# Optimization experiments

Measured on AMD Instinct MI355X. Metric: run time of the kernel, lower is better.

## Reference

```python
import jax, jax.numpy as jnp
import numpy as np

N, R, E, H, D_MAX = 1024, 8192, 1024, 4, 48
DH = E // H
P_EDGE = 16.0 / R  # average in-degree ~16


def setup_inputs() -> dict:
    key = jax.random.key(0)
    ks = jax.random.split(key, 6)
    s = 0.02
    return {
        "target": jax.random.normal(ks[0], (N, E), jnp.float32),
        "source": jax.random.normal(ks[1], (R, E), jnp.float32),
        "adj": (jax.random.uniform(ks[2], (N, R)) < P_EDGE).astype(jnp.float32),
        "W_trans": jax.random.normal(ks[3], (E, E), jnp.float32) * s,
        "b_trans": jnp.zeros((E,), jnp.float32),
        "in_proj_w": jax.random.normal(ks[4], (3 * E, E), jnp.float32) * s,
        "in_proj_b": jnp.zeros((3 * E,), jnp.float32),
        "out_w": jax.random.normal(ks[5], (E, E), jnp.float32) * s,
        "out_b": jnp.zeros((E,), jnp.float32),
        "unit_id": 0,
    }


def reference(target, source, adj, W_trans, b_trans, in_proj_w, in_proj_b, out_w, out_b, unit_id):
    # source = relu(trans_fc(source))
    src = jax.nn.relu(source @ W_trans.T + b_trans)  # [R, E]

    # build padded neighbor index lists (torch loops per node; here vectorized)
    deg = adj.sum(axis=1).astype(jnp.int32)                # [N]
    order = jnp.argsort(-adj, axis=1)[:, :D_MAX]           # stable: 1-columns first, ascending col idx
    valid = jnp.arange(D_MAX)[None, :] < deg[:, None]      # [N, D] True = real neighbor
    neigh = jnp.where(valid, order, 0)                     # pad with index 0 (masked, like torch)
    kv_in = src[neigh]                                     # [N, D, E] gathered neighbor feats

    # nn.MultiheadAttention: q=target (len-1 query), k=v=padded neighbors
    Wq, Wk, Wv = jnp.split(in_proj_w, 3, axis=0)
    bq, bk, bv = jnp.split(in_proj_b, 3)
    q = (target @ Wq.T + bq).reshape(-1, H, DH)            # [N, H, dh]
    k = (kv_in @ Wk.T + bk).reshape(-1, D_MAX, H, DH)      # [N, D, H, dh]
    v = (kv_in @ Wv.T + bv).reshape(-1, D_MAX, H, DH)

    scores = jnp.einsum('nhd,nkhd->nhk', q, k) / np.float32(np.sqrt(DH))  # [N, H, D]
    # key_padding_mask: padded slots -> -inf; give zero-degree nodes one dummy
    # unmasked slot so softmax stays finite (their output is zeroed below)
    safe_valid = valid.at[:, 0].set(valid[:, 0] | (deg == 0))
    scores = jnp.where(safe_valid[:, None, :], scores, -jnp.inf)
    attn = jax.nn.softmax(scores, axis=-1)
    out = jnp.einsum('nhk,nkhd->nhd', attn, v).reshape(-1, E)
    out = out @ out_w.T + out_b

    # scatter back: inactive (degree-0) nodes stay zero, like att_res_padded
    return jnp.where((deg > 0)[:, None], out, jnp.zeros((), out.dtype))
```

## Files before the change

kernel.cpp:

```cpp
#include <hip/hip_runtime.h>

#define N_NODES 1024
#define R_SRC   8192
#define E_DIM   1024
#define H_HEADS 4
#define DH_DIM  256
#define D_MAXN  48
#define NCONVB  1024

typedef __attribute__((ext_vector_type(8))) short short8;
typedef __attribute__((ext_vector_type(4))) float f32x4;

__device__ __forceinline__ unsigned short f2bf(float f) {
    unsigned u = __float_as_uint(f);
    unsigned r = u + 0x7fffu + ((u >> 16) & 1u);
    return (unsigned short)(r >> 16);
}
__device__ __forceinline__ float bf2f(unsigned short b) {
    return __uint_as_float(((unsigned)b) << 16);
}
__device__ __forceinline__ void gload16(const void* g, void* l) {
    __builtin_amdgcn_global_load_lds(
        (const __attribute__((address_space(1))) unsigned int*)g,
        (__attribute__((address_space(3))) unsigned int*)l,
        16, 0, 0);
}
template<int N> __device__ __forceinline__ void vwait() {
    if constexpr (N == 8)       asm volatile("s_waitcnt vmcnt(8)" ::: "memory");
    else if constexpr (N == 6)  asm volatile("s_waitcnt vmcnt(6)" ::: "memory");
    else if constexpr (N == 4)  asm volatile("s_waitcnt vmcnt(4)" ::: "memory");
    else if constexpr (N == 2)  asm volatile("s_waitcnt vmcnt(2)" ::: "memory");
    else                        asm volatile("s_waitcnt vmcnt(0)" ::: "memory");
}

struct GD {
    const unsigned short* A;
    const unsigned short* B;
    const float* bias;
    void* C;
    int N, K, nbx, relu, outbf;
    const int* rowmask;
};

template<int BM, int BN>
__global__ __launch_bounds__(512) void gemm_t(GD d0, GD d1, int split)
{
    constexpr int AI = BM / 64;
    constexpr int BI = BN / 64;
    constexpr int VN = AI + BI;
    constexpr int FM = BM / 32;
    constexpr int FN = BN / 64;

    __shared__ __align__(16) unsigned short lds[3][(BM + BN) * 64];

    int bid = blockIdx.x;
    const int nwg = gridDim.x;
    bid = (bid & 7) * (nwg >> 3) + (bid >> 3);

    GD d; int q;
    if (bid < split) { d = d0; q = bid; }
    else             { d = d1; q = bid - split; }
    const int m0 = (q / d.nbx) * BM;
    const int n0 = (q % d.nbx) * BN;
    const int K  = d.K;

    const int t = threadIdx.x;
    const int w = t >> 6, l = t & 63;
    const int wm = w >> 2, wn = w & 3;

    const int trow = t >> 3, tkc = t & 7;
    const int tswz = tkc ^ (trow & 7);
    const unsigned short* gA[AI];
    const unsigned short* gB[BI];
#pragma unroll
    for (int i = 0; i < AI; ++i)
        gA[i] = d.A + (size_t)(m0 + i * 64 + trow) * K + tswz * 8;
#pragma unroll
    for (int i = 0; i < BI; ++i)
        gB[i] = d.B + (size_t)(n0 + i * 64 + trow) * K + tswz * 8;

    f32x4 acc[FM][FN] = {};

    auto STAGE = [&](int c, int kt) {
        const int ko = kt * 64;
#pragma unroll
        for (int i = 0; i < AI; ++i)
            gload16(gA[i] + ko, &lds[c][(i * 512 + t) * 8]);
#pragma unroll
        for (int i = 0; i < BI; ++i)
            gload16(gB[i] + ko, &lds[c][BM * 64 + (i * 512 + t) * 8]);
    };

    const int nt = K / 64;
    STAGE(0, 0);
    STAGE(1, 1);
    vwait<VN>();
    __builtin_amdgcn_s_barrier();

    const int lr = l & 15, hi = l >> 4;
    const int rsw = l & 7;
    const int cs0 = ((0 + hi) ^ rsw) * 8;
    const int cs1 = ((4 + hi) ^ rsw) * 8;
    const int abase = (wm * (BM / 2) + lr) * 64;
    const int bbase = BM * 64 + (wn * 64 + lr) * 64;

    for (int kt = 0; kt < nt; ++kt) {
        const int cur = kt % 3;
        if (kt + 2 < nt) STAGE((kt + 2) % 3, kt + 2);

        const unsigned short* Ls = &lds[cur][0];

        short8 bv[FN][2];
#pragma unroll
        for (int fj = 0; fj < FN; ++fj) {
            bv[fj][0] = *(const short8*)&Ls[bbase + fj * 1024 + cs0];
            bv[fj][1] = *(const short8*)&Ls[bbase + fj * 1024 + cs1];
        }
#pragma unroll
        for (int g = 0; g < FM; g += 4) {
            short8 av[4][2];
#pragma unroll
            for (int fi = 0; fi < 4; ++fi) {
                av[fi][0] = *(const short8*)&Ls[abase + (g + fi) * 1024 + cs0];
                av[fi][1] = *(const short8*)&Ls[abase + (g + fi) * 1024 + cs1];
            }
            __builtin_amdgcn_s_setprio(1);
#pragma unroll
            for (int ks = 0; ks < 2; ++ks)
#pragma unroll
                for (int fi = 0; fi < 4; ++fi)
#pragma unroll
                    for (int fj = 0; fj < FN; ++fj)
                        acc[g + fi][fj] = __builtin_amdgcn_mfma_f32_16x16x32_bf16(
                            av[fi][ks], bv[fj][ks], acc[g + fi][fj], 0, 0, 0);
            __builtin_amdgcn_s_setprio(0);
        }

        asm volatile("" ::: "memory");
        __builtin_amdgcn_s_barrier();
        if (kt + 2 < nt) {
            vwait<VN>();
        } else {
            vwait<0>();
        }
        __builtin_amdgcn_s_barrier();
    }

#pragma unroll
    for (int fj = 0; fj < FN; ++fj) {
        const int c = n0 + wn * 64 + fj * 16 + lr;
        const float bvs = d.bias[c];
#pragma unroll
        for (int fi = 0; fi < FM; ++fi) {
            const int rb = m0 + wm * (BM / 2) + fi * 16 + hi * 4;
#pragma unroll
            for (int qq = 0; qq < 4; ++qq) {
                const int r = rb + qq;
                float x = acc[fi][fj][qq] + bvs;
                if (d.relu) x = fmaxf(x, 0.0f);
                if (d.rowmask && d.rowmask[r] == 0) x = 0.0f;
                if (d.outbf) ((unsigned short*)d.C)[(size_t)r * d.N + c] = f2bf(x);
                else         ((float*)d.C)[(size_t)r * d.N + c] = x;
            }
        }
    }
}

struct GS {
    const unsigned short* A;
    const unsigned short* B;
    const float* bias;
    void* C;
    int lda, ldb, ldc, K, relu, outbf;
    long long azs, bzs, czs;
    int bias_zs;
    const int* rowmask;
};

__global__ __launch_bounds__(256) void gemm_s(GS g)
{
    const int z = blockIdx.z;
    const unsigned short* A = g.A + (size_t)((long long)z * g.azs);
    const unsigned short* B = g.B + (size_t)((long long)z * g.bzs);
    const float* bias = g.bias ? g.bias + (size_t)z * g.bias_zs : nullptr;

    __shared__ __align__(16) unsigned short S[3][128 * 32];

    const int t = threadIdx.x;
    const int m0 = blockIdx.y * 64;
    const int n0 = blockIdx.x * 64;
    const int w = t >> 6, l = t & 63;
    const int wrow = (w >> 1) * 32;
    const int wcol = (w & 1) * 32;
    const int lr = l & 15;
    const int kg = (l >> 4) * 8;

    f32x4 acc[2][2] = {};

    const unsigned short* gp0 = A + (size_t)(m0 + (t >> 2)) * g.lda + (t & 3) * 8;
    const unsigned short* gp1 = B + (size_t)(n0 + (t >> 2)) * g.ldb + (t & 3) * 8;

    auto STAGE = [&](int c, int k0) {
        gload16(gp0 + k0, &S[c][t * 8]);
        gload16(gp1 + k0, &S[c][2048 + t * 8]);
    };

    const int nt = g.K / 32;
    STAGE(0, 0);
    STAGE(1, 32);
    vwait<2>();
    __builtin_amdgcn_s_barrier();

    for (int kt = 0; kt < nt; ++kt) {
        const int cur = kt % 3;
        if (kt + 2 < nt) STAGE((kt + 2) % 3, (kt + 2) * 32);

        const unsigned short* Ls = &S[cur][0];

        short8 af[2], bw[2];
#pragma unroll
        for (int i = 0; i < 2; ++i)
            af[i] = *(const short8*)&Ls[(wrow + i * 16 + lr) * 32 + kg];
#pragma unroll
        for (int j = 0; j < 2; ++j)
            bw[j] = *(const short8*)&Ls[2048 + (wcol + j * 16 + lr) * 32 + kg];
#pragma unroll
        for (int i = 0; i < 2; ++i)
#pragma unroll
            for (int j = 0; j < 2; ++j)
                acc[i][j] = __builtin_amdgcn_mfma_f32_16x16x32_bf16(
                    af[i], bw[j], acc[i][j], 0, 0, 0);

        asm volatile("" ::: "memory");
        __builtin_amdgcn_s_barrier();
        if (kt + 2 < nt) {
            vwait<2>();
        } else {
            vwait<0>();
        }
        __builtin_amdgcn_s_barrier();
    }

#pragma unroll
    for (int j = 0; j < 2; ++j) {
        const int c = n0 + wcol + j * 16 + lr;
        const float bv = bias ? bias[c] : 0.0f;
#pragma unroll
        for (int i = 0; i < 2; ++i) {
            const int rbase = m0 + wrow + i * 16 + (l >> 4) * 4;
#pragma unroll
            for (int qq = 0; qq < 4; ++qq) {
                const int r = rbase + qq;
                float x = acc[i][j][qq] + bv;
                if (g.relu) x = fmaxf(x, 0.0f);
                if (g.rowmask && g.rowmask[r] == 0) x = 0.0f;
                if (g.outbf)
                    ((unsigned short*)g.C)[(size_t)((long long)z * g.czs) + (size_t)r * g.ldc + c] = f2bf(x);
                else
                    ((float*)g.C)[(size_t)((long long)z * g.czs) + (size_t)r * g.ldc + c] = x;
            }
        }
    }
}

struct ConvArgs {
    const float* s[4];
    unsigned short* d[4];
    unsigned off[5];
};

__global__ __launch_bounds__(256) void pre_kernel(
    const float* __restrict__ adj, int* __restrict__ neigh, int* __restrict__ deg,
    ConvArgs a, const float* __restrict__ inw_f, const float* __restrict__ tgt_f,
    const float* __restrict__ in_b, unsigned short* __restrict__ WkT,
    unsigned short* __restrict__ Q_bf)
{
    __shared__ __align__(16) unsigned char smem[64 * 65 * 4];
    const int t = threadIdx.x;

    if (blockIdx.x < 256) {
        unsigned short (*QS)[64 * 32] = (unsigned short (*)[64 * 32])smem;
        const int qb = blockIdx.x;
        const int m0 = (qb >> 4) * 64;
        const int n0 = (qb & 15) * 64;
        const int w = t >> 6, l = t & 63;
        const int wrow = (w >> 1) * 32;
        const int wcol = (w & 1) * 32;
        const int lr = l & 15;
        const int kg = (l >> 4) * 8;
        const int row = t >> 2, k8 = (t & 3) * 8;

        const float* ga = tgt_f + (size_t)(m0 + row) * E_DIM + k8;
        const float* gb = inw_f + (size_t)(n0 + row) * E_DIM + k8;

        f32x4 acc[2][2] = {};

        for (int k0 = 0; k0 < E_DIM; k0 += 32) {
            float4 a0 = *(const float4*)(ga + k0);
            float4 a1 = *(const float4*)(ga + k0 + 4);
            float4 b0 = *(const float4*)(gb + k0);
            float4 b1 = *(const float4*)(gb + k0 + 4);
            short8 av, bv;
            av[0] = (short)f2bf(a0.x); av[1] = (short)f2bf(a0.y);
            av[2] = (short)f2bf(a0.z); av[3] = (short)f2bf(a0.w);
            av[4] = (short)f2bf(a1.x); av[5] = (short)f2bf(a1.y);
            av[6] = (short)f2bf(a1.z); av[7] = (short)f2bf(a1.w);
            bv[0] = (short)f2bf(b0.x); bv[1] = (short)f2bf(b0.y);
            bv[2] = (short)f2bf(b0.z); bv[3] = (short)f2bf(b0.w);
            bv[4] = (short)f2bf(b1.x); bv[5] = (short)f2bf(b1.y);
            bv[6] = (short)f2bf(b1.z); bv[7] = (short)f2bf(b1.w);
            *(short8*)&QS[0][row * 32 + k8] = av;
            *(short8*)&QS[1][row * 32 + k8] = bv;
            __syncthreads();

            short8 af[2], bw[2];
#pragma unroll
            for (int i = 0; i < 2; ++i)
                af[i] = *(const short8*)&QS[0][(wrow + i * 16 + lr) * 32 + kg];
#pragma unroll
            for (int j = 0; j < 2; ++j)
                bw[j] = *(const short8*)&QS[1][(wcol + j * 16 + lr) * 32 + kg];
#pragma unroll
            for (int i = 0; i < 2; ++i)
#pragma unroll
                for (int j = 0; j < 2; ++j)
                    acc[i][j] = __builtin_amdgcn_mfma_f32_16x16x32_bf16(
                        af[i], bw[j], acc[i][j], 0, 0, 0);
            __syncthreads();
        }

#pragma unroll
        for (int j = 0; j < 2; ++j) {
            const int c = n0 + wcol + j * 16 + lr;
            const float bv = in_b[c];
#pragma unroll
            for (int i = 0; i < 2; ++i) {
                const int rbase = m0 + wrow + i * 16 + (l >> 4) * 4;
#pragma unroll
                for (int qq = 0; qq < 4; ++qq)
                    Q_bf[(size_t)(rbase + qq) * E_DIM + c] = f2bf(acc[i][j][qq] + bv);
            }
        }
        return;
    }

    if (blockIdx.x < 512) {
        float (*tile)[65] = (float (*)[65])smem;
        const int tb = blockIdx.x - 256;
        const int h = tb >> 6, rem = tb & 63;
        const int e0 = (rem >> 2) * 64, d0 = (rem & 3) * 64;
        const int r = t >> 2, c4 = (t & 3) * 16;
        const float* tsrc = inw_f + (size_t)(E_DIM + h * 256 + d0 + r) * E_DIM + e0 + c4;
#pragma unroll
        for (int jj = 0; jj < 4; ++jj) {
            float4 v = ((const float4*)tsrc)[jj];
            tile[r][c4 + jj * 4 + 0] = v.x;
            tile[r][c4 + jj * 4 + 1] = v.y;
            tile[r][c4 + jj * 4 + 2] = v.z;
            tile[r][c4 + jj * 4 + 3] = v.w;
        }
        __syncthreads();
        const int er = t >> 2, dc = (t & 3) * 16;
        unsigned short* wout = WkT + ((size_t)h * E_DIM + e0 + er) * 256 + d0 + dc;
#pragma unroll
        for (int jj = 0; jj < 4; ++jj) {
            ushort4 o;
            o.x = f2bf(tile[dc + jj * 4 + 0][er]);
            o.y = f2bf(tile[dc + jj * 4 + 1][er]);
            o.z = f2bf(tile[dc + jj * 4 + 2][er]);
            o.w = f2bf(tile[dc + jj * 4 + 3][er]);
            ((ushort4*)wout)[jj] = o;
        }
        return;
    }

    if (blockIdx.x < (unsigned)(512 + N_NODES)) {
        int* s_cnt = (int*)smem;
        int (*s_idx)[D_MAXN] = (int (*)[D_MAXN])(smem + 16);

        const int n    = blockIdx.x - 512;
        const int w    = t >> 6;
        const int lane = t & 63;
        const float* row = adj + (size_t)n * R_SRC;

        const int seg0 = w * (R_SRC / 4);
        const unsigned long long lower = (1ULL << lane) - 1ULL;
        int total = 0;

        for (int base = seg0; base < seg0 + R_SRC / 4; base += 256) {
            const float4 v = *(const float4*)(row + base + lane * 4);
            const int b0 = (v.x != 0.0f), b1 = (v.y != 0.0f);
            const int b2 = (v.z != 0.0f), b3 = (v.w != 0.0f);
            const unsigned long long m0 = __ballot(b0);
            const unsigned long long m1 = __ballot(b1);
            const unsigned long long m2 = __ballot(b2);
            const unsigned long long m3 = __ballot(b3);
            int p = total + __popcll(m0 & lower) + __popcll(m1 & lower)
                          + __popcll(m2 & lower) + __popcll(m3 & lower);
            const int col = base + lane * 4;
            if (b0 && p < D_MAXN) s_idx[w][p] = col + 0;  p += b0;
            if (b1 && p < D_MAXN) s_idx[w][p] = col + 1;  p += b1;
            if (b2 && p < D_MAXN) s_idx[w][p] = col + 2;  p += b2;
            if (b3 && p < D_MAXN) s_idx[w][p] = col + 3;  p += b3;
            total += __popcll(m0) + __popcll(m1) + __popcll(m2) + __popcll(m3);
        }
        if (lane == 0) s_cnt[w] = total;
        __syncthreads();

        int start = 0;
#pragma unroll
        for (int i = 0; i < 4; ++i) if (i < w) start += s_cnt[i];
        const int degree = s_cnt[0] + s_cnt[1] + s_cnt[2] + s_cnt[3];
        const int nstore = total < D_MAXN ? total : D_MAXN;
        if (lane < nstore) {
            const int gpos = start + lane;
            if (gpos < D_MAXN) neigh[n * D_MAXN + gpos] = s_idx[w][lane];
        }
        if (t == 0) deg[n] = degree;
        return;
    }

    {
        const unsigned total = a.off[4];
        const unsigned stride = NCONVB * 2048;
        for (unsigned bs = (blockIdx.x - 512 - N_NODES) * 2048; bs < total; bs += stride) {
            float4 v[8];
            unsigned idx[8];
            int ok[8];
#pragma unroll
            for (int j = 0; j < 8; ++j) {
                idx[j] = bs + j * 256 + t;
                ok[j] = idx[j] < total;
            }
            int seg[8];
#pragma unroll
            for (int j = 0; j < 8; ++j) {
                seg[j] = 0;
#pragma unroll
                for (int s = 1; s < 4; ++s) seg[j] += (idx[j] >= a.off[s]);
            }
#pragma unroll
            for (int j = 0; j < 8; ++j)
                if (ok[j]) v[j] = ((const float4*)a.s[seg[j]])[idx[j] - a.off[seg[j]]];
#pragma unroll
            for (int j = 0; j < 8; ++j) {
                if (ok[j]) {
                    ushort4 o;
                    o.x = f2bf(v[j].x); o.y = f2bf(v[j].y);
                    o.z = f2bf(v[j].z); o.w = f2bf(v[j].w);
                    ((ushort4*)a.d[seg[j]])[idx[j] - a.off[seg[j]]] = o;
                }
            }
        }
    }
}

__global__ __launch_bounds__(256) void gather_ctx(
    const unsigned short* __restrict__ Ahat, const unsigned short* __restrict__ srcrel,
    const int* __restrict__ neigh, const int* __restrict__ deg,
    unsigned short* __restrict__ ctx)
{
    const int n = blockIdx.x;
    const int t = threadIdx.x;
    const int h = t >> 6;
    const int lane = t & 63;

    unsigned short* crow = ctx + ((size_t)n * H_HEADS + h) * E_DIM + lane * 16;
    const int degree = deg[n];
    if (degree == 0) {
        ushort4 z4 = {0, 0, 0, 0};
#pragma unroll
        for (int j = 0; j < 4; ++j) ((ushort4*)crow)[j] = z4;
        return;
    }
    const int dv = degree < D_MAXN ? degree : D_MAXN;

    __shared__ int s_neigh[D_MAXN];
    if (t < dv) s_neigh[t] = neigh[n * D_MAXN + t];
    __syncthreads();

    float a[16];
    {
        const short8* ap = (const short8*)(Ahat + ((size_t)n * H_HEADS + h) * E_DIM + lane * 16);
        short8 v0 = ap[0], v1 = ap[1];
#pragma unroll
        for (int j = 0; j < 8; ++j) {
            a[j]     = bf2f((unsigned short)v0[j]);
            a[8 + j] = bf2f((unsigned short)v1[j]);
        }
    }

    float m = -3.4e38f, sum = 0.0f;
    float cacc[16];
#pragma unroll
    for (int i = 0; i < 16; ++i) cacc[i] = 0.0f;

    const float scale = 0.0625f;

    int d = 0;
    for (; d + 1 < dv; d += 2) {
        const ushort4* rp0 = (const ushort4*)(srcrel + (size_t)s_neigh[d]     * E_DIM + lane * 16);
        const ushort4* rp1 = (const ushort4*)(srcrel + (size_t)s_neigh[d + 1] * E_DIM + lane * 16);
        ushort4 w00 = rp0[0], w01 = rp0[1], w02 = rp0[2], w03 = rp0[3];
        ushort4 w10 = rp1[0], w11 = rp1[1], w12 = rp1[2], w13 = rp1[3];
        float e0[16], e1[16];
        e0[0]=bf2f(w00.x); e0[1]=bf2f(w00.y); e0[2]=bf2f(w00.z); e0[3]=bf2f(w00.w);
        e0[4]=bf2f(w01.x); e0[5]=bf2f(w01.y); e0[6]=bf2f(w01.z); e0[7]=bf2f(w01.w);
        e0[8]=bf2f(w02.x); e0[9]=bf2f(w02.y); e0[10]=bf2f(w02.z); e0[11]=bf2f(w02.w);
        e0[12]=bf2f(w03.x); e0[13]=bf2f(w03.y); e0[14]=bf2f(w03.z); e0[15]=bf2f(w03.w);
        e1[0]=bf2f(w10.x); e1[1]=bf2f(w10.y); e1[2]=bf2f(w10.z); e1[3]=bf2f(w10.w);
        e1[4]=bf2f(w11.x); e1[5]=bf2f(w11.y); e1[6]=bf2f(w11.z); e1[7]=bf2f(w11.w);
        e1[8]=bf2f(w12.x); e1[9]=bf2f(w12.y); e1[10]=bf2f(w12.z); e1[11]=bf2f(w12.w);
        e1[12]=bf2f(w13.x); e1[13]=bf2f(w13.y); e1[14]=bf2f(w13.z); e1[15]=bf2f(w13.w);

        float s0 = 0.0f, s1 = 0.0f;
#pragma unroll
        for (int i = 0; i < 16; ++i) { s0 = fmaf(a[i], e0[i], s0); s1 = fmaf(a[i], e1[i], s1); }
#pragma unroll
        for (int off = 32; off > 0; off >>= 1) {
            s0 += __shfl_xor(s0, off);
            s1 += __shfl_xor(s1, off);
        }
        s0 *= scale; s1 *= scale;

        if (s0 > m) {
            const float f = __expf(m - s0);
            sum *= f;
#pragma unroll
            for (int i = 0; i < 16; ++i) cacc[i] *= f;
            m = s0;
        }
        {
            const float wgt = __expf(s0 - m);
            sum += wgt;
#pragma unroll
            for (int i = 0; i < 16; ++i) cacc[i] = fmaf(wgt, e0[i], cacc[i]);
        }
        if (s1 > m) {
            const float f = __expf(m - s1);
            sum *= f;
#pragma unroll
            for (int i = 0; i < 16; ++i) cacc[i] *= f;
            m = s1;
        }
        {
            const float wgt = __expf(s1 - m);
            sum += wgt;
#pragma unroll
            for (int i = 0; i < 16; ++i) cacc[i] = fmaf(wgt, e1[i], cacc[i]);
        }
    }
    for (; d < dv; ++d) {
        const ushort4* rp = (const ushort4*)(srcrel + (size_t)s_neigh[d] * E_DIM + lane * 16);
        float e[16];
#pragma unroll
        for (int j = 0; j < 4; ++j) {
            ushort4 v = rp[j];
            e[j * 4 + 0] = bf2f(v.x); e[j * 4 + 1] = bf2f(v.y);
            e[j * 4 + 2] = bf2f(v.z); e[j * 4 + 3] = bf2f(v.w);
        }
        float s = 0.0f;
#pragma unroll
        for (int i = 0; i < 16; ++i) s = fmaf(a[i], e[i], s);
#pragma unroll
        for (int off = 32; off > 0; off >>= 1) s += __shfl_xor(s, off);
        s *= scale;
        if (s > m) {
            const float f = __expf(m - s);
            sum *= f;
#pragma unroll
            for (int i = 0; i < 16; ++i) cacc[i] *= f;
            m = s;
        }
        const float wgt = __expf(s - m);
        sum += wgt;
#pragma unroll
        for (int i = 0; i < 16; ++i) cacc[i] = fmaf(wgt, e[i], cacc[i]);
    }

    const float inv = 1.0f / sum;
#pragma unroll
    for (int j = 0; j < 4; ++j) {
        ushort4 o;
        o.x = f2bf(cacc[j * 4 + 0] * inv);
        o.y = f2bf(cacc[j * 4 + 1] * inv);
        o.z = f2bf(cacc[j * 4 + 2] * inv);
        o.w = f2bf(cacc[j * 4 + 3] * inv);
        ((ushort4*)crow)[j] = o;
    }
}

extern "C" void kernel_launch(void* const* d_in, const int* in_sizes, int n_in,
                              void* d_out, int out_size, void* d_ws, size_t ws_size,
                              hipStream_t stream)
{
    const float* target  = (const float*)d_in[0];
    const float* source  = (const float*)d_in[1];
    const float* adj     = (const float*)d_in[2];
    const float* W_trans = (const float*)d_in[3];
    const float* b_trans = (const float*)d_in[4];
    const float* in_w    = (const float*)d_in[5];
    const float* in_b    = (const float*)d_in[6];
    const float* out_w   = (const float*)d_in[7];
    const float* out_b   = (const float*)d_in[8];
    float* out = (float*)d_out;

    char* ws = (char*)d_ws;
    unsigned short* src_bf    = (unsigned short*)ws; ws += (size_t)R_SRC * E_DIM * 2;
    unsigned short* wt_bf     = (unsigned short*)ws; ws += (size_t)E_DIM * E_DIM * 2;
    unsigned short* wv_bf     = (unsigned short*)ws; ws += (size_t)E_DIM * E_DIM * 2;
    unsigned short* outw_bf   = (unsigned short*)ws; ws += (size_t)E_DIM * E_DIM * 2;
    unsigned short* srcrel_bf = (unsigned short*)ws; ws += (size_t)R_SRC * E_DIM * 2;
    unsigned short* WkT_bf    = (unsigned short*)ws; ws += (size_t)H_HEADS * E_DIM * DH_DIM * 2;
    unsigned short* Q_bf      = (unsigned short*)ws; ws += (size_t)N_NODES * E_DIM * 2;
    unsigned short* Ahat_bf   = (unsigned short*)ws; ws += (size_t)N_NODES * H_HEADS * E_DIM * 2;
    unsigned short* ctx_bf    = (unsigned short*)ws; ws += (size_t)N_NODES * H_HEADS * E_DIM * 2;
    unsigned short* attn_bf   = (unsigned short*)ws; ws += (size_t)N_NODES * E_DIM * 2;
    int*            neigh     = (int*)ws;            ws += (size_t)N_NODES * D_MAXN * 4;
    int*            deg       = (int*)ws;            ws += (size_t)N_NODES * 4;

    const size_t EE = (size_t)E_DIM * E_DIM;

    {
        ConvArgs a;
        const unsigned sz4[4] = {
            (unsigned)((size_t)R_SRC * E_DIM / 4),
            (unsigned)(EE / 4),
            (unsigned)(EE / 4),
            (unsigned)(EE / 4)};
        a.s[0] = source;        a.d[0] = src_bf;
        a.s[1] = W_trans;       a.d[1] = wt_bf;
        a.s[2] = in_w + 2 * EE; a.d[2] = wv_bf;
        a.s[3] = out_w;         a.d[3] = outw_bf;
        a.off[0] = 0;
        for (int i = 0; i < 4; ++i) a.off[i + 1] = a.off[i] + sz4[i];
        pre_kernel<<<512 + N_NODES + NCONVB, 256, 0, stream>>>(
            adj, neigh, deg, a, in_w, target, in_b, WkT_bf, Q_bf);
    }

    {
        GD ds;
        ds.A = src_bf; ds.B = wt_bf; ds.bias = b_trans; ds.C = srcrel_bf;
        ds.N = E_DIM; ds.K = E_DIM; ds.nbx = E_DIM / 256; ds.relu = 1; ds.outbf = 1;
        ds.rowmask = nullptr;
        const int sblocks = (R_SRC / 128) * (E_DIM / 256);
        gemm_t<128, 256><<<sblocks, 512, 0, stream>>>(ds, ds, sblocks);
    }

    {
        GS g;
        g.A = Q_bf; g.B = WkT_bf; g.bias = nullptr; g.C = Ahat_bf;
        g.lda = E_DIM; g.ldb = DH_DIM; g.ldc = H_HEADS * E_DIM; g.K = DH_DIM;
        g.relu = 0; g.outbf = 1;
        g.azs = DH_DIM;
        g.bzs = (long long)E_DIM * DH_DIM;
        g.czs = E_DIM;
        g.bias_zs = 0; g.rowmask = nullptr;
        gemm_s<<<dim3(E_DIM / 64, N_NODES / 64, H_HEADS), 256, 0, stream>>>(g);
    }

    gather_ctx<<<N_NODES, 256, 0, stream>>>(Ahat_bf, srcrel_bf, neigh, deg, ctx_bf);

    {
        GS g;
        g.A = ctx_bf; g.B = wv_bf; g.bias = in_b + 2 * E_DIM; g.C = attn_bf;
        g.lda = H_HEADS * E_DIM; g.ldb = E_DIM; g.ldc = E_DIM; g.K = E_DIM;
        g.relu = 0; g.outbf = 1;
        g.azs = E_DIM;
        g.bzs = (long long)DH_DIM * E_DIM;
        g.czs = DH_DIM;
        g.bias_zs = DH_DIM; g.rowmask = nullptr;
        gemm_s<<<dim3(DH_DIM / 64, N_NODES / 64, H_HEADS), 256, 0, stream>>>(g);
    }

    {
        GS g;
        g.A = attn_bf; g.B = outw_bf; g.bias = out_b; g.C = out;
        g.lda = E_DIM; g.ldb = E_DIM; g.ldc = E_DIM; g.K = E_DIM;
        g.relu = 0; g.outbf = 0; g.azs = 0; g.bzs = 0; g.czs = 0; g.bias_zs = 0;
        g.rowmask = deg;
        gemm_s<<<dim3(E_DIM / 64, N_NODES / 64, 1), 256, 0, stream>>>(g);
    }
}
```

Before: 104.1 us.

## Move Q projection out of pre_kernel into separate bf16 GEMM launch

The Q = target @ Wq^T projection used to run inside pre_kernel as 256 blocks that loaded fp32 and converted to bf16 on every k-step. Now target and Wq are converted to bf16 by the existing bulk conversion path, and Q is computed by the generic gemm_s kernel in a separate launch. pre_kernel's block layout is reordered so the adjacency and WkT transpose blocks come first. This trades an extra kernel launch and extra bf16 workspace traffic for a cleaner GEMM that does no per-step conversion and shortens pre_kernel.

```diff
diff --git a/kernel.cpp b/kernel.cpp
--- a/kernel.cpp
+++ b/kernel.cpp
@@ -264,121 +264,23 @@
 }
 
 struct ConvArgs {
-    const float* s[4];
-    unsigned short* d[4];
-    unsigned off[5];
+    const float* s[6];
+    unsigned short* d[6];
+    unsigned off[7];
 };
 
 __global__ __launch_bounds__(256) void pre_kernel(
     const float* __restrict__ adj, int* __restrict__ neigh, int* __restrict__ deg,
-    ConvArgs a, const float* __restrict__ inw_f, const float* __restrict__ tgt_f,
-    const float* __restrict__ in_b, unsigned short* __restrict__ WkT,
-    unsigned short* __restrict__ Q_bf)
+    ConvArgs a, const float* __restrict__ inw_f, unsigned short* __restrict__ WkT)
 {
     __shared__ __align__(16) unsigned char smem[64 * 65 * 4];
     const int t = threadIdx.x;
 
-    if (blockIdx.x < 256) {
-        unsigned short (*QS)[64 * 32] = (unsigned short (*)[64 * 32])smem;
-        const int qb = blockIdx.x;
-        const int m0 = (qb >> 4) * 64;
-        const int n0 = (qb & 15) * 64;
-        const int w = t >> 6, l = t & 63;
-        const int wrow = (w >> 1) * 32;
-        const int wcol = (w & 1) * 32;
-        const int lr = l & 15;
-        const int kg = (l >> 4) * 8;
-        const int row = t >> 2, k8 = (t & 3) * 8;
-
-        const float* ga = tgt_f + (size_t)(m0 + row) * E_DIM + k8;
-        const float* gb = inw_f + (size_t)(n0 + row) * E_DIM + k8;
-
-        f32x4 acc[2][2] = {};
-
-        for (int k0 = 0; k0 < E_DIM; k0 += 32) {
-            float4 a0 = *(const float4*)(ga + k0);
-            float4 a1 = *(const float4*)(ga + k0 + 4);
-            float4 b0 = *(const float4*)(gb + k0);
-            float4 b1 = *(const float4*)(gb + k0 + 4);
-            short8 av, bv;
-            av[0] = (short)f2bf(a0.x); av[1] = (short)f2bf(a0.y);
-            av[2] = (short)f2bf(a0.z); av[3] = (short)f2bf(a0.w);
-            av[4] = (short)f2bf(a1.x); av[5] = (short)f2bf(a1.y);
-            av[6] = (short)f2bf(a1.z); av[7] = (short)f2bf(a1.w);
-            bv[0] = (short)f2bf(b0.x); bv[1] = (short)f2bf(b0.y);
-            bv[2] = (short)f2bf(b0.z); bv[3] = (short)f2bf(b0.w);
-            bv[4] = (short)f2bf(b1.x); bv[5] = (short)f2bf(b1.y);
-            bv[6] = (short)f2bf(b1.z); bv[7] = (short)f2bf(b1.w);
-            *(short8*)&QS[0][row * 32 + k8] = av;
-            *(short8*)&QS[1][row * 32 + k8] = bv;
-            __syncthreads();
-
-            short8 af[2], bw[2];
-#pragma unroll
-            for (int i = 0; i < 2; ++i)
-                af[i] = *(const short8*)&QS[0][(wrow + i * 16 + lr) * 32 + kg];
-#pragma unroll
-            for (int j = 0; j < 2; ++j)
-                bw[j] = *(const short8*)&QS[1][(wcol + j * 16 + lr) * 32 + kg];
-#pragma unroll
-            for (int i = 0; i < 2; ++i)
-#pragma unroll
-                for (int j = 0; j < 2; ++j)
-                    acc[i][j] = __builtin_amdgcn_mfma_f32_16x16x32_bf16(
-                        af[i], bw[j], acc[i][j], 0, 0, 0);
-            __syncthreads();
-        }
-
-#pragma unroll
-        for (int j = 0; j < 2; ++j) {
-            const int c = n0 + wcol + j * 16 + lr;
-            const float bv = in_b[c];
-#pragma unroll
-            for (int i = 0; i < 2; ++i) {
-                const int rbase = m0 + wrow + i * 16 + (l >> 4) * 4;
-#pragma unroll
-                for (int qq = 0; qq < 4; ++qq)
-                    Q_bf[(size_t)(rbase + qq) * E_DIM + c] = f2bf(acc[i][j][qq] + bv);
-            }
-        }
-        return;
-    }
-
-    if (blockIdx.x < 512) {
-        float (*tile)[65] = (float (*)[65])smem;
-        const int tb = blockIdx.x - 256;
-        const int h = tb >> 6, rem = tb & 63;
-        const int e0 = (rem >> 2) * 64, d0 = (rem & 3) * 64;
-        const int r = t >> 2, c4 = (t & 3) * 16;
-        const float* tsrc = inw_f + (size_t)(E_DIM + h * 256 + d0 + r) * E_DIM + e0 + c4;
-#pragma unroll
-        for (int jj = 0; jj < 4; ++jj) {
-            float4 v = ((const float4*)tsrc)[jj];
-            tile[r][c4 + jj * 4 + 0] = v.x;
-            tile[r][c4 + jj * 4 + 1] = v.y;
-            tile[r][c4 + jj * 4 + 2] = v.z;
-            tile[r][c4 + jj * 4 + 3] = v.w;
-        }
-        __syncthreads();
-        const int er = t >> 2, dc = (t & 3) * 16;
-        unsigned short* wout = WkT + ((size_t)h * E_DIM + e0 + er) * 256 + d0 + dc;
-#pragma unroll
-        for (int jj = 0; jj < 4; ++jj) {
-            ushort4 o;
-            o.x = f2bf(tile[dc + jj * 4 + 0][er]);
-            o.y = f2bf(tile[dc + jj * 4 + 1][er]);
-            o.z = f2bf(tile[dc + jj * 4 + 2][er]);
-            o.w = f2bf(tile[dc + jj * 4 + 3][er]);
-            ((ushort4*)wout)[jj] = o;
-        }
-        return;
-    }
-
-    if (blockIdx.x < (unsigned)(512 + N_NODES)) {
+    if (blockIdx.x < N_NODES) {
         int* s_cnt = (int*)smem;
         int (*s_idx)[D_MAXN] = (int (*)[D_MAXN])(smem + 16);
 
-        const int n    = blockIdx.x - 512;
+        const int n    = blockIdx.x;
         const int w    = t >> 6;
         const int lane = t & 63;
         const float* row = adj + (size_t)n * R_SRC;
@@ -420,10 +322,40 @@
         return;
     }
 
-    {
-        const unsigned total = a.off[4];
+    if (blockIdx.x < (unsigned)(N_NODES + 256)) {
+        float (*tile)[65] = (float (*)[65])smem;
+        const int tb = blockIdx.x - N_NODES;
+        const int h = tb >> 6, rem = tb & 63;
+        const int e0 = (rem >> 2) * 64, d0 = (rem & 3) * 64;
+        const int r = t >> 2, c4 = (t & 3) * 16;
+        const float* tsrc = inw_f + (size_t)(E_DIM + h * 256 + d0 + r) * E_DIM + e0 + c4;
+#pragma unroll
+        for (int jj = 0; jj < 4; ++jj) {
+            float4 v = ((const float4*)tsrc)[jj];
+            tile[r][c4 + jj * 4 + 0] = v.x;
+            tile[r][c4 + jj * 4 + 1] = v.y;
+            tile[r][c4 + jj * 4 + 2] = v.z;
+            tile[r][c4 + jj * 4 + 3] = v.w;
+        }
+        __syncthreads();
+        const int er = t >> 2, dc = (t & 3) * 16;
+        unsigned short* wout = WkT + ((size_t)h * E_DIM + e0 + er) * 256 + d0 + dc;
+#pragma unroll
+        for (int jj = 0; jj < 4; ++jj) {
+            ushort4 o;
+            o.x = f2bf(tile[dc + jj * 4 + 0][er]);
+            o.y = f2bf(tile[dc + jj * 4 + 1][er]);
+            o.z = f2bf(tile[dc + jj * 4 + 2][er]);
+            o.w = f2bf(tile[dc + jj * 4 + 3][er]);
+            ((ushort4*)wout)[jj] = o;
+        }
+        return;
+    }
+
+    {
+        const unsigned total = a.off[6];
         const unsigned stride = NCONVB * 2048;
-        for (unsigned bs = (blockIdx.x - 512 - N_NODES) * 2048; bs < total; bs += stride) {
+        for (unsigned bs = (blockIdx.x - N_NODES - 256) * 2048; bs < total; bs += stride) {
             float4 v[8];
             unsigned idx[8];
             int ok[8];
@@ -437,7 +369,7 @@
             for (int j = 0; j < 8; ++j) {
                 seg[j] = 0;
 #pragma unroll
-                for (int s = 1; s < 4; ++s) seg[j] += (idx[j] >= a.off[s]);
+                for (int s = 1; s < 6; ++s) seg[j] += (idx[j] >= a.off[s]);
             }
 #pragma unroll
             for (int j = 0; j < 8; ++j)
@@ -610,6 +542,8 @@
     unsigned short* wt_bf     = (unsigned short*)ws; ws += (size_t)E_DIM * E_DIM * 2;
     unsigned short* wv_bf     = (unsigned short*)ws; ws += (size_t)E_DIM * E_DIM * 2;
     unsigned short* outw_bf   = (unsigned short*)ws; ws += (size_t)E_DIM * E_DIM * 2;
+    unsigned short* wq_bf     = (unsigned short*)ws; ws += (size_t)E_DIM * E_DIM * 2;
+    unsigned short* tgt_bf    = (unsigned short*)ws; ws += (size_t)N_NODES * E_DIM * 2;
     unsigned short* srcrel_bf = (unsigned short*)ws; ws += (size_t)R_SRC * E_DIM * 2;
     unsigned short* WkT_bf    = (unsigned short*)ws; ws += (size_t)H_HEADS * E_DIM * DH_DIM * 2;
     unsigned short* Q_bf      = (unsigned short*)ws; ws += (size_t)N_NODES * E_DIM * 2;
@@ -623,19 +557,32 @@
 
     {
         ConvArgs a;
-        const unsigned sz4[4] = {
+        const unsigned sz4[6] = {
             (unsigned)((size_t)R_SRC * E_DIM / 4),
             (unsigned)(EE / 4),
             (unsigned)(EE / 4),
-            (unsigned)(EE / 4)};
+            (unsigned)(EE / 4),
+            (unsigned)(EE / 4),
+            (unsigned)((size_t)N_NODES * E_DIM / 4)};
         a.s[0] = source;        a.d[0] = src_bf;
         a.s[1] = W_trans;       a.d[1] = wt_bf;
         a.s[2] = in_w + 2 * EE; a.d[2] = wv_bf;
         a.s[3] = out_w;         a.d[3] = outw_bf;
+        a.s[4] = in_w;          a.d[4] = wq_bf;
+        a.s[5] = target;        a.d[5] = tgt_bf;
         a.off[0] = 0;
-        for (int i = 0; i < 4; ++i) a.off[i + 1] = a.off[i] + sz4[i];
-        pre_kernel<<<512 + N_NODES + NCONVB, 256, 0, stream>>>(
-            adj, neigh, deg, a, in_w, target, in_b, WkT_bf, Q_bf);
+        for (int i = 0; i < 6; ++i) a.off[i + 1] = a.off[i] + sz4[i];
+        pre_kernel<<<N_NODES + 256 + NCONVB, 256, 0, stream>>>(
+            adj, neigh, deg, a, in_w, WkT_bf);
+    }
+
+    {
+        GS g;
+        g.A = tgt_bf; g.B = wq_bf; g.bias = in_b; g.C = Q_bf;
+        g.lda = E_DIM; g.ldb = E_DIM; g.ldc = E_DIM; g.K = E_DIM;
+        g.relu = 0; g.outbf = 1;
+        g.azs = 0; g.bzs = 0; g.czs = 0; g.bias_zs = 0; g.rowmask = nullptr;
+        gemm_s<<<dim3(E_DIM / 64, N_NODES / 64, 1), 256, 0, stream>>>(g);
     }
 
     {
```

After: 109.3 us. 1.05x slower.
